# Kernel optimization log

Hardware: AMD Instinct MI355X
Metric: run time of the kernel (lower is better)

## Reference

```python
import jax, jax.numpy as jnp
import numpy as np

N_NODES = 100000
N_EDGES = 800000
DIM_E = 64
HEAD = 4


def setup_inputs() -> dict:
    key = jax.random.key(0)
    ks = jax.random.split(key, 6)
    embeds = jax.random.normal(ks[0], (N_NODES, DIM_E), dtype=jnp.float32)
    Wq = jax.random.normal(ks[1], (DIM_E, DIM_E), dtype=jnp.float32) * (1.0 / np.sqrt(DIM_E))
    Wk = jax.random.normal(ks[2], (DIM_E, DIM_E), dtype=jnp.float32) * (1.0 / np.sqrt(DIM_E))
    Wv = jax.random.normal(ks[3], (DIM_E, DIM_E), dtype=jnp.float32) * (1.0 / np.sqrt(DIM_E))
    rows = jax.random.randint(ks[4], (N_EDGES,), 0, N_NODES, dtype=jnp.int32)
    cols = jax.random.randint(ks[5], (N_EDGES,), 0, N_NODES, dtype=jnp.int32)
    return {"embeds": embeds, "Wq": Wq, "Wk": Wk, "Wv": Wv, "rows": rows, "cols": cols}


def reference(embeds, Wq, Wk, Wv, rows, cols):
    H, D = HEAD, DIM_E
    Dh = D // H
    E = rows.shape[0]
    rowE = embeds[rows]                     # [E, D] gather
    colE = embeds[cols]                     # [E, D] gather
    q = (rowE @ Wq).reshape(E, H, Dh)
    k = (colE @ Wk).reshape(E, H, Dh)
    v = (colE @ Wv).reshape(E, H, Dh)
    att = jnp.clip(jnp.einsum('ehd,ehd->eh', q, k), -10.0, 10.0)
    expAtt = jnp.exp(att)                   # [E, H]
    # segment softmax: scatter-add per destination row, gather back
    attNorm = jax.ops.segment_sum(expAtt, rows, num_segments=N_NODES)[rows]
    att = expAtt / (attNorm + 1e-8)         # [E, H]
    res = (att[:, :, None] * v).reshape(E, D)
    res = jax.ops.segment_sum(res, rows, num_segments=N_NODES)  # [N, D]
    return (res, att)
```

## Files before the change

kernel.cpp:

```cpp
#include <hip/hip_runtime.h>

#define N_NODES 100000
#define N_EDGES 800000
#define DIM 64
#define HEADS 4

#define SCAN_BLK 256
#define N_SCAN_BLOCKS ((N_NODES + SCAN_BLK - 1) / SCAN_BLK)

typedef __attribute__((ext_vector_type(8))) short bf16x8;
typedef __attribute__((ext_vector_type(4))) float f32x4;

__device__ __forceinline__ short f2bf(float x) {
    union { float f; unsigned u; } v; v.f = x;
    unsigned r = (v.u + 0x7FFFu + ((v.u >> 16) & 1u)) >> 16;
    return (short)r;
}
__device__ __forceinline__ float bf2f(short b) {
    union { float f; unsigned u; } v; v.u = ((unsigned)(unsigned short)b) << 16;
    return v.f;
}

__global__ __launch_bounds__(256) void wprep_kernel(
    const float* __restrict__ Wq, const float* __restrict__ Wk,
    const float* __restrict__ Wv,
    short* __restrict__ wfragH, short* __restrict__ wfragL)
{
    const int idx = blockIdx.x * 256 + threadIdx.x;
    if (idx >= 12288) return;
    const int j    = idx & 7;
    const int lane = (idx >> 3) & 63;
    const int kt   = (idx >> 9) & 1;
    const int nt   = idx >> 10;
    const int k      = kt * 32 + (lane >> 4) * 8 + j;
    const int col192 = nt * 16 + (lane & 15);
    const float* W = (col192 < 64) ? Wq : ((col192 < 128) ? Wk : Wv);
    const float x = W[k * DIM + (col192 & 63)];
    const short hb = f2bf(x);
    wfragH[idx] = hb;
    wfragL[idx] = f2bf(x - bf2f(hb));
}

__global__ __launch_bounds__(256) void qkv_mfma_kernel(
    const float* __restrict__ embeds,
    const short* __restrict__ wfragH,
    const short* __restrict__ wfragL,
    float* __restrict__ Q,
    unsigned short* __restrict__ Kb,
    unsigned short* __restrict__ Vb)
{
    __shared__ __align__(16) short sBH[12288];
    __shared__ __align__(16) short sBL[12288];

    const int t = threadIdx.x;
    {
        const int4* srcH = (const int4*)wfragH;
        const int4* srcL = (const int4*)wfragL;
        int4* dH = (int4*)sBH; int4* dL = (int4*)sBL;
        #pragma unroll
        for (int i = 0; i < 6; ++i) {
            dH[t + 256 * i] = srcH[t + 256 * i];
            dL[t + 256 * i] = srcL[t + 256 * i];
        }
    }
    __syncthreads();

    const int lane = t & 63;
    const int wid  = t >> 6;
    const int m0 = blockIdx.x * 64 + wid * 16;

    int arow = m0 + (lane & 15);
    if (arow >= N_NODES) arow = N_NODES - 1;
    const float* ap = embeds + (size_t)arow * DIM + ((lane >> 4) * 8);

    bf16x8 aH[2], aL[2];
    #pragma unroll
    for (int kt = 0; kt < 2; ++kt) {
        const float4 x0 = ((const float4*)(ap + kt * 32))[0];
        const float4 x1 = ((const float4*)(ap + kt * 32))[1];
        const float xs[8] = {x0.x, x0.y, x0.z, x0.w, x1.x, x1.y, x1.z, x1.w};
        bf16x8 h8, l8;
        #pragma unroll
        for (int j = 0; j < 8; ++j) {
            const short hb = f2bf(xs[j]);
            h8[j] = hb;
            l8[j] = f2bf(xs[j] - bf2f(hb));
        }
        aH[kt] = h8; aL[kt] = l8;
    }

    f32x4 acc[12];
    #pragma unroll
    for (int nt = 0; nt < 12; ++nt) acc[nt] = (f32x4){0.f, 0.f, 0.f, 0.f};

    #pragma unroll
    for (int kt = 0; kt < 2; ++kt) {
        #pragma unroll
        for (int nt = 0; nt < 12; ++nt) {
            const int o = ((nt * 2 + kt) * 64 + lane) * 8;
            const bf16x8 bH = *(const bf16x8*)(sBH + o);
            const bf16x8 bL = *(const bf16x8*)(sBL + o);
            acc[nt] = __builtin_amdgcn_mfma_f32_16x16x32_bf16(aH[kt], bH, acc[nt], 0, 0, 0);
            acc[nt] = __builtin_amdgcn_mfma_f32_16x16x32_bf16(aH[kt], bL, acc[nt], 0, 0, 0);
            acc[nt] = __builtin_amdgcn_mfma_f32_16x16x32_bf16(aL[kt], bH, acc[nt], 0, 0, 0);
        }
    }

    const int rbase = m0 + (lane >> 4) * 4;
    const int cl = lane & 15;
    #pragma unroll
    for (int nt = 0; nt < 12; ++nt) {
        const int col192 = nt * 16 + cl;
        #pragma unroll
        for (int r = 0; r < 4; ++r) {
            const int row = rbase + r;
            if (row < N_NODES) {
                if (col192 < 64)
                    Q[(size_t)row * DIM + col192] = acc[nt][r];
                else if (col192 < 128)
                    Kb[(size_t)row * DIM + (col192 - 64)] = (unsigned short)f2bf(acc[nt][r]);
                else
                    Vb[(size_t)row * DIM + (col192 - 128)] = (unsigned short)f2bf(acc[nt][r]);
            }
        }
    }
}

__global__ __launch_bounds__(256) void hist_kernel(
    const int* __restrict__ rows, int* __restrict__ counts,
    int* __restrict__ rank)
{
    const int e = blockIdx.x * 256 + threadIdx.x;
    if (e < N_EDGES) rank[e] = atomicAdd(&counts[rows[e]], 1);
}

__global__ __launch_bounds__(SCAN_BLK) void scanA_kernel(
    const int* __restrict__ counts, int* __restrict__ blockSums)
{
    __shared__ int tile[SCAN_BLK];
    const int i = blockIdx.x * SCAN_BLK + threadIdx.x;
    tile[threadIdx.x] = (i < N_NODES) ? counts[i] : 0;
    __syncthreads();
    for (int off = SCAN_BLK / 2; off > 0; off >>= 1) {
        if (threadIdx.x < off) tile[threadIdx.x] += tile[threadIdx.x + off];
        __syncthreads();
    }
    if (threadIdx.x == 0) blockSums[blockIdx.x] = tile[0];
}

__global__ __launch_bounds__(512) void scanB_kernel(int* __restrict__ blockSums)
{
    __shared__ int s[512];
    const int t = threadIdx.x;
    const int v = (t < N_SCAN_BLOCKS) ? blockSums[t] : 0;
    s[t] = v;
    __syncthreads();
    for (int off = 1; off < 512; off <<= 1) {
        const int add = (t >= off) ? s[t - off] : 0;
        __syncthreads();
        s[t] += add;
        __syncthreads();
    }
    if (t < N_SCAN_BLOCKS) blockSums[t] = s[t] - v;
}

__global__ __launch_bounds__(SCAN_BLK) void scanC_kernel(
    const int* __restrict__ counts,
    const int* __restrict__ blockSums,
    int* __restrict__ offsets)
{
    __shared__ int tile[SCAN_BLK];
    const int i = blockIdx.x * SCAN_BLK + threadIdx.x;
    const int v = (i < N_NODES) ? counts[i] : 0;
    tile[threadIdx.x] = v;
    __syncthreads();
    for (int off = 1; off < SCAN_BLK; off <<= 1) {
        const int add = (threadIdx.x >= off) ? tile[threadIdx.x - off] : 0;
        __syncthreads();
        tile[threadIdx.x] += add;
        __syncthreads();
    }
    if (i < N_NODES) offsets[i] = tile[threadIdx.x] - v + blockSums[blockIdx.x];
}

__global__ __launch_bounds__(256) void scatter_kernel(
    const int* __restrict__ rows,
    const int* __restrict__ cols,
    const int* __restrict__ offsets,
    const int* __restrict__ rank,
    int2* __restrict__ sortedPair)
{
    const int e = blockIdx.x * 256 + threadIdx.x;
    if (e < N_EDGES) {
        const int pos = offsets[rows[e]] + rank[e];
        sortedPair[pos] = make_int2(cols[e], e);
    }
}

__global__ __launch_bounds__(256) void node_agg_kernel(
    const float* __restrict__ Q,
    const unsigned short* __restrict__ Kb,
    const unsigned short* __restrict__ Vb,
    const int* __restrict__ offsets,
    const int* __restrict__ counts,
    const int2* __restrict__ sortedPair,
    float* __restrict__ attOut,
    float* __restrict__ normArr,
    float* __restrict__ res)
{
    const int node = (blockIdx.x * 256 + threadIdx.x) >> 6;
    const int lane = threadIdx.x & 63;
    if (node >= N_NODES) return;

    const int start = offsets[node];
    const int cnt   = counts[node];

    const int slot = lane >> 2;
    const int h    = lane & 3;
    const int hd   = lane >> 4;

    float qv[16];
    {
        const float4* qp = (const float4*)(Q + (size_t)node * DIM + h * 16);
        ((float4*)qv)[0] = qp[0]; ((float4*)qv)[1] = qp[1];
        ((float4*)qv)[2] = qp[2]; ((float4*)qv)[3] = qp[3];
    }

    float normacc = 0.0f;
    float acc     = 0.0f;

    for (int cb = 0; cb < cnt; cb += 16) {
        const int jj = cb + slot;
        const bool active = (jj < cnt);
        int2 pr = make_int2(0, 0);
        if (active) pr = sortedPair[start + jj];
        const int col = pr.x;

        const unsigned short* kp = Kb + (size_t)col * DIM + h * 16;
        const bf16x8 k0 = *(const bf16x8*)kp;
        const bf16x8 k1 = *(const bf16x8*)(kp + 8);
        float s = 0.0f;
        #pragma unroll
        for (int j = 0; j < 8; ++j) s = fmaf(qv[j], bf2f(k0[j]), s);
        #pragma unroll
        for (int j = 0; j < 8; ++j) s = fmaf(qv[8 + j], bf2f(k1[j]), s);

        s = fminf(fmaxf(s, -10.0f), 10.0f);
        const float ex = active ? __expf(s) : 0.0f;
        if (active) attOut[(size_t)pr.y * HEADS + h] = ex;
        normacc += ex;

        unsigned short raw[16];
        #pragma unroll
        for (int s2 = 0; s2 < 16; ++s2) {
            const int c2 = __builtin_amdgcn_readlane(col, s2 * 4);
            raw[s2] = Vb[(size_t)c2 * DIM + lane];
        }
        #pragma unroll
        for (int s2 = 0; s2 < 16; ++s2) {
            acc = fmaf(__shfl(ex, s2 * 4 + hd, 64), bf2f((short)raw[s2]), acc);
        }
    }

    #pragma unroll
    for (int m2 = 4; m2 <= 32; m2 <<= 1)
        normacc += __shfl_xor(normacc, m2, 64);

    if (lane < 4) normArr[(size_t)node * HEADS + lane] = normacc;

    const float nrm = __shfl(normacc, hd, 64);
    res[(size_t)node * DIM + lane] = acc / (nrm + 1e-8f);
}

__global__ __launch_bounds__(256) void norm_edge_kernel(
    const int* __restrict__ rows,
    const float* __restrict__ normArr,
    float* __restrict__ attOut)
{
    const int e = blockIdx.x * 256 + threadIdx.x;
    if (e >= N_EDGES) return;
    float4 ex4 = ((const float4*)attOut)[e];
    const float4 n4 = ((const float4*)normArr)[rows[e]];
    ex4.x /= (n4.x + 1e-8f);
    ex4.y /= (n4.y + 1e-8f);
    ex4.z /= (n4.z + 1e-8f);
    ex4.w /= (n4.w + 1e-8f);
    ((float4*)attOut)[e] = ex4;
}


extern "C" void kernel_launch(void* const* d_in, const int* in_sizes, int n_in,
                              void* d_out, int out_size, void* d_ws, size_t ws_size,
                              hipStream_t stream) {
    const float* embeds = (const float*)d_in[0];
    const float* Wq     = (const float*)d_in[1];
    const float* Wk     = (const float*)d_in[2];
    const float* Wv     = (const float*)d_in[3];
    const int*   rows   = (const int*)d_in[4];
    const int*   cols   = (const int*)d_in[5];

    float* out    = (float*)d_out;
    float* res    = out;
    float* attOut = out + (size_t)N_NODES * DIM;

    float*          Q         = (float*)d_ws;
    unsigned short* Kb        = (unsigned short*)(Q + (size_t)N_NODES * DIM);
    unsigned short* Vb        = Kb + (size_t)N_NODES * DIM;
    int2*           sortedPair= (int2*)(Vb + (size_t)N_NODES * DIM);
    int*            counts    = (int*)(sortedPair + N_EDGES);
    int*            offsets   = counts + N_NODES;
    int*            rank      = offsets + N_NODES;
    int*            blockSums = rank + N_EDGES;
    short*          wfragH    = (short*)(blockSums + 512);
    short*          wfragL    = wfragH + 12288;
    float*          normArr   = (float*)(wfragL + 12288);

    hipMemsetAsync(counts, 0, (size_t)N_NODES * sizeof(int), stream);

    wprep_kernel<<<48, 256, 0, stream>>>(Wq, Wk, Wv, wfragH, wfragL);
    qkv_mfma_kernel<<<(N_NODES + 63) / 64, 256, 0, stream>>>(embeds, wfragH, wfragL, Q, Kb, Vb);

    const int eblocks = (N_EDGES + 255) / 256;
    hist_kernel<<<eblocks, 256, 0, stream>>>(rows, counts, rank);
    scanA_kernel<<<N_SCAN_BLOCKS, SCAN_BLK, 0, stream>>>(counts, blockSums);
    scanB_kernel<<<1, 512, 0, stream>>>(blockSums);
    scanC_kernel<<<N_SCAN_BLOCKS, SCAN_BLK, 0, stream>>>(counts, blockSums, offsets);
    scatter_kernel<<<eblocks, 256, 0, stream>>>(rows, cols, offsets, rank, sortedPair);

    const int nblocks = (N_NODES * 64 + 255) / 256;
    node_agg_kernel<<<nblocks, 256, 0, stream>>>(Q, Kb, Vb, offsets, counts,
                                                 sortedPair, attOut, normArr, res);

    norm_edge_kernel<<<eblocks, 256, 0, stream>>>(rows, normArr, attOut);
}
```

Measured before the change: 231.5 us.

## Store exp scores in CSR order, split K dot across half-waves, fold scanB into scanC

The node aggregation kernel now processes 8 edges per iteration, with the two half-waves each computing half of the 16-wide head dot product and combining them with a shuffle. This halves K loads per lane and register use. Exp scores are written contiguously in CSR order instead of scattered by edge id, and the normalization kernel gathers them back through a position array written during the scatter. The separate single-block scanB launch is removed, so every scanC block redundantly scans the block sums itself. This trades one launch for duplicated work and adds an extra per-edge position array and an indirect read.

Measured after the change: 232.7 us. Within noise of the previous version (+0.5%).

```diff
diff --git a/kernel.cpp b/kernel.cpp
--- a/kernel.cpp
+++ b/kernel.cpp
@@ -148,39 +148,43 @@
     if (threadIdx.x == 0) blockSums[blockIdx.x] = tile[0];
 }
 
-__global__ __launch_bounds__(512) void scanB_kernel(int* __restrict__ blockSums)
-{
-    __shared__ int s[512];
-    const int t = threadIdx.x;
-    const int v = (t < N_SCAN_BLOCKS) ? blockSums[t] : 0;
-    s[t] = v;
-    __syncthreads();
-    for (int off = 1; off < 512; off <<= 1) {
-        const int add = (t >= off) ? s[t - off] : 0;
-        __syncthreads();
-        s[t] += add;
-        __syncthreads();
-    }
-    if (t < N_SCAN_BLOCKS) blockSums[t] = s[t] - v;
-}
-
 __global__ __launch_bounds__(SCAN_BLK) void scanC_kernel(
     const int* __restrict__ counts,
     const int* __restrict__ blockSums,
     int* __restrict__ offsets)
 {
+    __shared__ int pairs[256];
     __shared__ int tile[SCAN_BLK];
-    const int i = blockIdx.x * SCAN_BLK + threadIdx.x;
+    __shared__ int sPrefix;
+    const int t = threadIdx.x;
+
+    const int i0 = 2 * t, i1 = 2 * t + 1;
+    const int a = (i0 < N_SCAN_BLOCKS) ? blockSums[i0] : 0;
+    const int b = (i1 < N_SCAN_BLOCKS) ? blockSums[i1] : 0;
+    pairs[t] = a + b;
+    __syncthreads();
+    for (int off = 1; off < 256; off <<= 1) {
+        const int add = (t >= off) ? pairs[t - off] : 0;
+        __syncthreads();
+        pairs[t] += add;
+        __syncthreads();
+    }
+    if (t == (blockIdx.x >> 1)) {
+        const int pexcl = pairs[t] - (a + b);
+        sPrefix = pexcl + ((blockIdx.x & 1) ? a : 0);
+    }
+
+    const int i = blockIdx.x * SCAN_BLK + t;
     const int v = (i < N_NODES) ? counts[i] : 0;
-    tile[threadIdx.x] = v;
+    tile[t] = v;
     __syncthreads();
     for (int off = 1; off < SCAN_BLK; off <<= 1) {
-        const int add = (threadIdx.x >= off) ? tile[threadIdx.x - off] : 0;
-        __syncthreads();
-        tile[threadIdx.x] += add;
-        __syncthreads();
-    }
-    if (i < N_NODES) offsets[i] = tile[threadIdx.x] - v + blockSums[blockIdx.x];
+        const int add = (t >= off) ? tile[t - off] : 0;
+        __syncthreads();
+        tile[t] += add;
+        __syncthreads();
+    }
+    if (i < N_NODES) offsets[i] = tile[t] - v + sPrefix;
 }
 
 __global__ __launch_bounds__(256) void scatter_kernel(
@@ -188,12 +192,14 @@
     const int* __restrict__ cols,
     const int* __restrict__ offsets,
     const int* __restrict__ rank,
-    int2* __restrict__ sortedPair)
+    int* __restrict__ sortedCol,
+    int* __restrict__ posArr)
 {
     const int e = blockIdx.x * 256 + threadIdx.x;
     if (e < N_EDGES) {
         const int pos = offsets[rows[e]] + rank[e];
-        sortedPair[pos] = make_int2(cols[e], e);
+        sortedCol[pos] = cols[e];
+        posArr[e] = pos;
     }
 }
 
@@ -203,8 +209,8 @@
     const unsigned short* __restrict__ Vb,
     const int* __restrict__ offsets,
     const int* __restrict__ counts,
-    const int2* __restrict__ sortedPair,
-    float* __restrict__ attOut,
+    const int* __restrict__ sortedCol,
+    float* __restrict__ expCsr,
     float* __restrict__ normArr,
     float* __restrict__ res)
 {
@@ -215,55 +221,51 @@
     const int start = offsets[node];
     const int cnt   = counts[node];
 
-    const int slot = lane >> 2;
     const int h    = lane & 3;
+    const int slot = (lane >> 2) & 7;
+    const int half = lane >> 5;
     const int hd   = lane >> 4;
 
-    float qv[16];
+    float qv[8];
     {
-        const float4* qp = (const float4*)(Q + (size_t)node * DIM + h * 16);
-        ((float4*)qv)[0] = qp[0]; ((float4*)qv)[1] = qp[1];
-        ((float4*)qv)[2] = qp[2]; ((float4*)qv)[3] = qp[3];
+        const float4* qp = (const float4*)(Q + (size_t)node * DIM + h * 16 + half * 8);
+        ((float4*)qv)[0] = qp[0];
+        ((float4*)qv)[1] = qp[1];
     }
 
     float normacc = 0.0f;
     float acc     = 0.0f;
 
-    for (int cb = 0; cb < cnt; cb += 16) {
+    for (int cb = 0; cb < cnt; cb += 8) {
         const int jj = cb + slot;
         const bool active = (jj < cnt);
-        int2 pr = make_int2(0, 0);
-        if (active) pr = sortedPair[start + jj];
-        const int col = pr.x;
-
-        const unsigned short* kp = Kb + (size_t)col * DIM + h * 16;
-        const bf16x8 k0 = *(const bf16x8*)kp;
-        const bf16x8 k1 = *(const bf16x8*)(kp + 8);
+        int col = 0;
+        if (active) col = sortedCol[start + jj];
+
+        const bf16x8 k8 = *(const bf16x8*)(Kb + (size_t)col * DIM + h * 16 + half * 8);
         float s = 0.0f;
         #pragma unroll
-        for (int j = 0; j < 8; ++j) s = fmaf(qv[j], bf2f(k0[j]), s);
-        #pragma unroll
-        for (int j = 0; j < 8; ++j) s = fmaf(qv[8 + j], bf2f(k1[j]), s);
-
+        for (int j = 0; j < 8; ++j) s = fmaf(qv[j], bf2f(k8[j]), s);
+        s += __shfl_xor(s, 32, 64);
         s = fminf(fmaxf(s, -10.0f), 10.0f);
         const float ex = active ? __expf(s) : 0.0f;
-        if (active) attOut[(size_t)pr.y * HEADS + h] = ex;
+        if (active && half == 0) expCsr[(size_t)(start + jj) * HEADS + h] = ex;
         normacc += ex;
 
-        unsigned short raw[16];
-        #pragma unroll
-        for (int s2 = 0; s2 < 16; ++s2) {
+        unsigned short raw[8];
+        #pragma unroll
+        for (int s2 = 0; s2 < 8; ++s2) {
             const int c2 = __builtin_amdgcn_readlane(col, s2 * 4);
             raw[s2] = Vb[(size_t)c2 * DIM + lane];
         }
         #pragma unroll
-        for (int s2 = 0; s2 < 16; ++s2) {
+        for (int s2 = 0; s2 < 8; ++s2) {
             acc = fmaf(__shfl(ex, s2 * 4 + hd, 64), bf2f((short)raw[s2]), acc);
         }
     }
 
     #pragma unroll
-    for (int m2 = 4; m2 <= 32; m2 <<= 1)
+    for (int m2 = 4; m2 <= 16; m2 <<= 1)
         normacc += __shfl_xor(normacc, m2, 64);
 
     if (lane < 4) normArr[(size_t)node * HEADS + lane] = normacc;
@@ -274,12 +276,15 @@
 
 __global__ __launch_bounds__(256) void norm_edge_kernel(
     const int* __restrict__ rows,
+    const int* __restrict__ posArr,
+    const float* __restrict__ expCsr,
     const float* __restrict__ normArr,
     float* __restrict__ attOut)
 {
     const int e = blockIdx.x * 256 + threadIdx.x;
     if (e >= N_EDGES) return;
-    float4 ex4 = ((const float4*)attOut)[e];
+    const int p = posArr[e];
+    float4 ex4 = ((const float4*)expCsr)[p];
     const float4 n4 = ((const float4*)normArr)[rows[e]];
     ex4.x /= (n4.x + 1e-8f);
     ex4.y /= (n4.y + 1e-8f);
@@ -306,14 +311,16 @@
     float*          Q         = (float*)d_ws;
     unsigned short* Kb        = (unsigned short*)(Q + (size_t)N_NODES * DIM);
     unsigned short* Vb        = Kb + (size_t)N_NODES * DIM;
-    int2*           sortedPair= (int2*)(Vb + (size_t)N_NODES * DIM);
-    int*            counts    = (int*)(sortedPair + N_EDGES);
+    float*          expCsr    = (float*)(Vb + (size_t)N_NODES * DIM);
+    float*          normArr   = expCsr + (size_t)N_EDGES * HEADS;
+    int*            sortedCol = (int*)(normArr + (size_t)N_NODES * HEADS);
+    int*            posArr    = sortedCol + N_EDGES;
+    int*            rank      = posArr + N_EDGES;
+    int*            counts    = rank + N_EDGES;
     int*            offsets   = counts + N_NODES;
-    int*            rank      = offsets + N_NODES;
-    int*            blockSums = rank + N_EDGES;
+    int*            blockSums = offsets + N_NODES;
     short*          wfragH    = (short*)(blockSums + 512);
     short*          wfragL    = wfragH + 12288;
-    float*          normArr   = (float*)(wfragL + 12288);
 
     hipMemsetAsync(counts, 0, (size_t)N_NODES * sizeof(int), stream);
 
@@ -323,13 +330,12 @@
     const int eblocks = (N_EDGES + 255) / 256;
     hist_kernel<<<eblocks, 256, 0, stream>>>(rows, counts, rank);
     scanA_kernel<<<N_SCAN_BLOCKS, SCAN_BLK, 0, stream>>>(counts, blockSums);
-    scanB_kernel<<<1, 512, 0, stream>>>(blockSums);
     scanC_kernel<<<N_SCAN_BLOCKS, SCAN_BLK, 0, stream>>>(counts, blockSums, offsets);
-    scatter_kernel<<<eblocks, 256, 0, stream>>>(rows, cols, offsets, rank, sortedPair);
+    scatter_kernel<<<eblocks, 256, 0, stream>>>(rows, cols, offsets, rank, sortedCol, posArr);
 
     const int nblocks = (N_NODES * 64 + 255) / 256;
     node_agg_kernel<<<nblocks, 256, 0, stream>>>(Q, Kb, Vb, offsets, counts,
-                                                 sortedPair, attOut, normArr, res);
-
-    norm_edge_kernel<<<eblocks, 256, 0, stream>>>(rows, normArr, attOut);
-}
+                                                 sortedCol, expCsr, normArr, res);
+
+    norm_edge_kernel<<<eblocks, 256, 0, stream>>>(rows, posArr, expCsr, normArr, attOut);
+}
```
